# Kernel tuning notes

Hardware: AMD Instinct MI355X
Metric: run time of the kernel (lower is better)

Reference implementation:

```python
import jax, jax.numpy as jnp
import numpy as np

N_QUBITS = 14
N_TROTTER = 10
EVO_TIME = 1.0
BATCH = 2048
DIM = 2 ** N_QUBITS

# (-1)**bit_q(idx) for every basis index (Qiskit little-endian: qubit q <-> bit q)
_bits = (np.arange(DIM)[:, None] >> np.arange(N_QUBITS)[None, :]) & 1
_SIGNS = np.asarray(1 - 2 * _bits, dtype=np.float32)  # (DIM, n)


def _apply_1q(psi, U, q, n):
    A = 2 ** (n - 1 - q)
    B = 2 ** q
    psi = psi.reshape(A, 2, B)
    psi = jnp.einsum('ij,ajb->aib', U, psi)
    return psi.reshape(-1)


def _apply_zz(psi, theta, q, n):
    # CX(q,q+1); RZ(theta) on q+1; CX(q,q+1)  ==  diagonal exp(-i*theta/2 * Z_q Z_{q+1})
    A = 2 ** (n - 2 - q)
    B = 2 ** q
    em = jnp.exp(-0.5j * theta)
    ep = jnp.exp(0.5j * theta)
    diag = jnp.stack([em, ep, ep, em])  # axis index = 2*bit_{q+1} + bit_q
    psi = psi.reshape(A, 4, B) * diag[None, :, None]
    return psi.reshape(-1)


def _base_state(J, g):
    # Fixed part of the circuit (same for every sample): H on all qubits, then Trotter steps.
    n = N_QUBITS
    dt = EVO_TIME / N_TROTTER
    inv = 1.0 / np.sqrt(2.0)
    H = jnp.array([[inv, inv], [inv, -inv]], dtype=jnp.complex64)
    psi = jnp.zeros(DIM, dtype=jnp.complex64).at[0].set(1.0)
    for q in range(n):
        psi = _apply_1q(psi, H, q, n)
    for _ in range(N_TROTTER):
        for i in range(n - 1):
            psi = _apply_zz(psi, J[i] * dt, i, n)
        for i in range(n):
            half = 0.5 * g[i] * dt
            c = jnp.cos(half).astype(jnp.complex64)
            ms = -1j * jnp.sin(half)
            RX = jnp.stack([jnp.stack([c, ms]), jnp.stack([ms, c])])
            psi = _apply_1q(psi, RX, i, n)
    return psi


def _expectations(psi):
    # psi: (batch, DIM). Original observable order: block i -> qubit n-1-i, [X, Y, Z].
    n = N_QUBITS
    outs = []
    for i in range(n):
        q = n - 1 - i
        A = 2 ** (n - 1 - q)
        B = 2 ** q
        pr = psi.reshape(-1, A, 2, B)
        p0 = pr[:, :, 0, :]
        p1 = pr[:, :, 1, :]
        c = jnp.sum(jnp.conj(p0) * p1, axis=(1, 2))
        outs.append(2.0 * jnp.real(c))  # <X_q>
        outs.append(2.0 * jnp.imag(c))  # <Y_q>
        outs.append(jnp.sum(p0.real ** 2 + p0.imag ** 2 - p1.real ** 2 - p1.imag ** 2, axis=(1, 2)))  # <Z_q>
    return jnp.stack(outs, axis=1).astype(jnp.float32)


def setup_inputs() -> dict:
    key = jax.random.key(0)
    kx, kj, kg = jax.random.split(key, 3)
    x = jax.random.normal(kx, (BATCH, N_QUBITS), dtype=jnp.float32)
    J = jax.random.uniform(kj, (N_QUBITS - 1,), minval=0.5, maxval=1.5, dtype=jnp.float32)
    g = jax.random.uniform(kg, (N_QUBITS,), minval=0.5, maxval=1.5, dtype=jnp.float32)
    return {"x": x, "J": J, "g": g}


def reference(x, J, g):
    psi0 = _base_state(J, g)  # (DIM,), shared across the batch
    S = jnp.asarray(_SIGNS)   # (DIM, n)
    # Final per-sample RZ(x[b,q]) on qubit q -> diagonal phase exp(-i/2 * sum_q x_q * (-1)^bit_q)
    phase = jnp.exp((-0.5j) * (x @ S.T).astype(jnp.complex64))  # (batch, DIM)
    psi = psi0[None, :] * phase
    return _expectations(psi)
```

## Files before the change

### kernel.cpp

```cpp
#include <hip/hip_runtime.h>

#define NQ     14
#define DIMQ   16384
#define NWG    16
#define NTHR   256

typedef float vfloat4 __attribute__((ext_vector_type(4)));

struct Smem {
    float2 slab0[1024];
    float2 slab1[1024];
    float2 tabLo[64];
    float2 tabHi[128];
    float  red[48];
};

__device__ __forceinline__ void ld8v(const float2* p, float rb, float2 r[4]) {
    vfloat4 a, b;
    for (;;) {
        asm volatile("global_load_dwordx4 %0, %2, off sc0 sc1\n\t"
                     "global_load_dwordx4 %1, %2, off offset:16 sc0 sc1\n\t"
                     "s_waitcnt vmcnt(0)"
                     : "=&v"(a), "=&v"(b) : "v"(p) : "memory");
        float m0 = fminf(fminf(a.x * rb, a.y * rb), fminf(a.z * rb, a.w * rb));
        float m1 = fminf(fminf(b.x * rb, b.y * rb), fminf(b.z * rb, b.w * rb));
        bool ok = fminf(m0, m1) > 8.0f;
        if (__ballot(!ok) == 0ull) break;
        __builtin_amdgcn_s_sleep(1);
    }
    r[0] = make_float2(a.x - rb, a.y - rb); r[1] = make_float2(a.z - rb, a.w - rb);
    r[2] = make_float2(b.x - rb, b.y - rb); r[3] = make_float2(b.z - rb, b.w - rb);
}
__device__ __forceinline__ float2 d2f2(double d) { union { double d; float2 f; } u; u.d = d; return u.f; }
__device__ __forceinline__ double f22d(float2 f) { union { double d; float2 f; } u; u.f = f; return u.d; }
__device__ __forceinline__ void st2b(float2* p, float2 v, float wb) {
    float2 e = make_float2(v.x + wb, v.y + wb);
    asm volatile("global_store_dwordx2 %0, %1, off sc0 sc1"
                 : : "v"(p), "v"(f22d(e)) : "memory");
}
__device__ __forceinline__ void st8b(float2* p, const float2 r[4], float wb) {
    vfloat4 a, b;
    a.x = r[0].x + wb; a.y = r[0].y + wb; a.z = r[1].x + wb; a.w = r[1].y + wb;
    b.x = r[2].x + wb; b.y = r[2].y + wb; b.z = r[3].x + wb; b.w = r[3].y + wb;
    asm volatile("global_store_dwordx4 %0, %1, off sc0 sc1\n\t"
                 "global_store_dwordx4 %0, %2, off offset:16 sc0 sc1"
                 : : "v"(p), "v"(a), "v"(b) : "memory");
}
__device__ __forceinline__ void stfb(float* p, float v, float wb) {
    float e = v + wb;
    asm volatile("global_store_dword %0, %1, off sc0 sc1" : : "v"(p), "v"(e) : "memory");
}
__device__ __forceinline__ void ld3v(const float* p, float rb, bool use2,
                                     float& r0, float& r1, float& r2) {
    for (;;) {
        asm volatile("global_load_dword %0, %3, off sc0 sc1\n\t"
                     "global_load_dword %1, %3, off offset:1024 sc0 sc1\n\t"
                     "global_load_dword %2, %3, off offset:2048 sc0 sc1\n\t"
                     "s_waitcnt vmcnt(0)"
                     : "=&v"(r0), "=&v"(r1), "=&v"(r2) : "v"(p) : "memory");
        float m = fminf(r0 * rb, r1 * rb);
        if (use2) m = fminf(m, r2 * rb);
        bool ok = m > 8.0f;
        if (__ballot(!ok) == 0ull) break;
        __builtin_amdgcn_s_sleep(1);
    }
    r0 -= rb; r1 -= rb; r2 -= rb;
}

__device__ __forceinline__ float2 cmulf(float2 a, float2 b) {
    return make_float2(a.x * b.x - a.y * b.y, a.x * b.y + a.y * b.x);
}
__device__ __forceinline__ void bfly(float2& p0, float2& p1, float c, float s) {
    float2 n0 = make_float2(c * p0.x + s * p1.y, c * p0.y - s * p1.x);
    float2 n1 = make_float2(c * p1.x + s * p0.y, c * p1.y - s * p0.x);
    p0 = n0; p1 = n1;
}
__device__ __forceinline__ void bfly_shfl(float2& p, int mask, float c, float s) {
    float qx = __shfl_xor(p.x, mask);
    float qy = __shfl_xor(p.y, mask);
    p = make_float2(c * p.x + s * qy, c * p.y - s * qx);
}
__device__ __forceinline__ void zz_apply(const Smem& sm, float2& a, int k) {
    int d = (k ^ (k >> 1)) & 0x1FFF;
    float2 rot = cmulf(sm.tabLo[d & 63], sm.tabHi[d >> 6]);
    a = cmulf(a, rot);
}
__device__ __forceinline__ void stage_12(float2* slab, float2 r[4], int t) {
#pragma unroll
    for (int j = 0; j < 4; ++j) slab[(t << 2) | j] = r[j];
    __syncthreads();
#pragma unroll
    for (int j = 0; j < 4; ++j) r[j] = slab[t | (j << 8)];
}
__device__ __forceinline__ void stage_21(float2* slab, float2 r[4], int t) {
#pragma unroll
    for (int j = 0; j < 4; ++j) slab[t | (j << 8)] = r[j];
    __syncthreads();
#pragma unroll
    for (int j = 0; j < 4; ++j) r[j] = slab[(t << 2) | j];
}
__device__ __forceinline__ void reduce_qubit(const float2* slab, float* red,
                                             int sb, int i, int t) {
    float cr = 0.f, ci = 0.f, z = 0.f;
#pragma unroll
    for (int j = 0; j < 4; ++j) {
        const int m = (t << 2) | j;
        const float2 a = slab[m];
        const float n = a.x * a.x + a.y * a.y;
        if ((m >> sb) & 1) {
            z -= n;
        } else {
            z += n;
            const float2 b = slab[m ^ (1 << sb)];
            cr += a.x * b.x + a.y * b.y;
            ci += a.x * b.y - a.y * b.x;
        }
    }
#pragma unroll
    for (int off = 32; off; off >>= 1) {
        cr += __shfl_down(cr, off);
        ci += __shfl_down(ci, off);
        z  += __shfl_down(z, off);
    }
    if ((t & 63) == 0) {
        atomicAdd(&red[3 * i + 0], cr);
        atomicAdd(&red[3 * i + 1], ci);
        atomicAdd(&red[3 * i + 2], z);
    }
}

template <bool FIRST>
__device__ void phaseA(Smem& sm, float2* slab, float2* psi, int w, int t,
                       const float* c, const float* s, float rb, float wb) {
    float2 r[4];
    if (FIRST) {
#pragma unroll
        for (int j = 0; j < 4; ++j) r[j] = make_float2(0.0078125f, 0.0f);
    } else {
        ld8v(&psi[(w << 10) | (t << 2)], rb, r);
#pragma unroll
        for (int b = 2; b < 6; ++b) {
#pragma unroll
            for (int j = 0; j < 4; ++j) bfly_shfl(r[j], 1 << b, c[2 + b], s[2 + b]);
        }
    }
#pragma unroll
    for (int j = 0; j < 4; ++j) zz_apply(sm, r[j], (w << 10) | (t << 2) | j);
    bfly(r[0], r[1], c[0], s[0]); bfly(r[2], r[3], c[0], s[0]);
    bfly(r[0], r[2], c[1], s[1]); bfly(r[1], r[3], c[1], s[1]);
#pragma unroll
    for (int b = 0; b < 6; ++b) {
#pragma unroll
        for (int j = 0; j < 4; ++j) bfly_shfl(r[j], 1 << b, c[2 + b], s[2 + b]);
    }
    stage_12(slab, r, t);
    bfly(r[0], r[1], c[8], s[8]); bfly(r[2], r[3], c[8], s[8]);
    bfly(r[0], r[2], c[9], s[9]); bfly(r[1], r[3], c[9], s[9]);
#pragma unroll
    for (int j = 0; j < 4; ++j) st2b(&psi[(w << 10) | t | (j << 8)], r[j], wb);
}

template <bool KEEPSLAB>
__device__ void phaseB(Smem& sm, float2* s12, float2* s21, float2* psi,
                       int w, int t, const float* c, const float* s,
                       float rb, float wb) {
    float2 r[4];
    const int kbase = ((t >> 2) << 8) | (w << 4) | ((t & 3) << 2);
    ld8v(&psi[kbase], rb, r);
#pragma unroll
    for (int j = 0; j < 4; ++j) bfly_shfl(r[j], 16, c[10], s[10]);
#pragma unroll
    for (int j = 0; j < 4; ++j) bfly_shfl(r[j], 32, c[11], s[11]);
    stage_12(s12, r, t);
    bfly(r[0], r[1], c[12], s[12]); bfly(r[2], r[3], c[12], s[12]);
    bfly(r[0], r[2], c[13], s[13]); bfly(r[1], r[3], c[13], s[13]);
#pragma unroll
    for (int j = 0; j < 4; ++j) {
        const int m = t | (j << 8);
        zz_apply(sm, r[j], ((m >> 4) << 8) | (w << 4) | (m & 15));
    }
    bfly(r[0], r[1], c[12], s[12]); bfly(r[2], r[3], c[12], s[12]);
    bfly(r[0], r[2], c[13], s[13]); bfly(r[1], r[3], c[13], s[13]);
#pragma unroll
    for (int b = 0; b < 4; ++b) {
#pragma unroll
        for (int j = 0; j < 4; ++j) bfly_shfl(r[j], 1 << b, c[b], s[b]);
    }
#pragma unroll
    for (int j = 0; j < 4; ++j) bfly_shfl(r[j], 16, c[8], s[8]);
#pragma unroll
    for (int j = 0; j < 4; ++j) bfly_shfl(r[j], 32, c[9], s[9]);
    stage_21(s21, r, t);
#pragma unroll
    for (int j = 0; j < 4; ++j) bfly_shfl(r[j], 16, c[10], s[10]);
#pragma unroll
    for (int j = 0; j < 4; ++j) bfly_shfl(r[j], 32, c[11], s[11]);
    st8b(&psi[kbase], r, wb);
    if (KEEPSLAB) {
#pragma unroll
        for (int j = 0; j < 4; ++j) s21[(t << 2) | j] = r[j];
    }
}

extern "C" __global__ void __launch_bounds__(NTHR)
qr_all(const float* __restrict__ x, const float* __restrict__ J,
       const float* __restrict__ g, float* __restrict__ out,
       float2* __restrict__ psi, float* __restrict__ P) {
    __shared__ Smem sm;
    const int w = blockIdx.x;
    const int t = threadIdx.x;
    const float dt = 0.1f;

    if (t < 64) {
        float phi = 0.0f;
        for (int i = 0; i < 6; ++i) {
            const float h = 0.5f * J[i] * dt;
            phi += ((t >> i) & 1) ? h : -h;
        }
        float sn, cs; __sincosf(phi, &sn, &cs);
        sm.tabLo[t] = make_float2(cs, sn);
    } else if (t < 192) {
        const int v = t - 64;
        float phi = 0.0f;
        for (int i = 0; i < 7; ++i) {
            const float h = 0.5f * J[6 + i] * dt;
            phi += ((v >> i) & 1) ? h : -h;
        }
        float sn, cs; __sincosf(phi, &sn, &cs);
        sm.tabHi[v] = make_float2(cs, sn);
    }
    if (t < 48) sm.red[t] = 0.0f;
    float cc[NQ], ss[NQ];
#pragma unroll
    for (int i = 0; i < NQ; ++i) __sincosf(0.5f * g[i] * dt, &ss[i], &cc[i]);
    __syncthreads();

    phaseA<true>(sm, sm.slab0, psi, w, t, cc, ss, 0.0f, -4.0f);

    float esn[7], ecs[7];
#pragma unroll
    for (int k = 0; k < 7; ++k) {
        const int task = w * NTHR + t + (k << 12);
        const int b = task / NQ;
        const int i = task - b * NQ;
        __sincosf(x[b * NQ + 13 - i], &esn[k], &ecs[k]);
    }

#pragma unroll 1
    for (int sstep = 1; sstep <= 9; ++sstep) {
        const float wb = ((sstep + 1) & 1) ? -4.0f : 4.0f;
        const float rb = -wb;
        if (sstep & 1) {
            const int i21 = ((sstep - 1) >> 1) & 1;
            float2* s21 = i21 ? sm.slab1 : sm.slab0;
            float2* s12 = i21 ? sm.slab0 : sm.slab1;
            if (sstep == 9) {
                phaseB<true>(sm, s12, s21, psi, w, t, cc, ss, rb, wb);
                __syncthreads();
#pragma unroll
                for (int q = 0; q <= 3; ++q) reduce_qubit(sm.slab0, sm.red, q, 13 - q, t);
#pragma unroll
                for (int q = 8; q <= 13; ++q) reduce_qubit(sm.slab0, sm.red, q - 4, 13 - q, t);
            } else {
                phaseB<false>(sm, s12, s21, psi, w, t, cc, ss, rb, wb);
            }
        } else {
            float2* slab = ((sstep >> 1) & 1) ? sm.slab1 : sm.slab0;
            phaseA<false>(sm, slab, psi, w, t, cc, ss, rb, wb);
        }
    }

    {
        float2 r[4];
        ld8v(&psi[(w << 10) | (t << 2)], 4.0f, r);
#pragma unroll
        for (int b = 2; b < 6; ++b) {
#pragma unroll
            for (int j = 0; j < 4; ++j) bfly_shfl(r[j], 1 << b, cc[2 + b], ss[2 + b]);
        }
#pragma unroll
        for (int j = 0; j < 4; ++j) sm.slab1[(t << 2) | j] = r[j];
        __syncthreads();
#pragma unroll
        for (int q = 4; q <= 7; ++q) reduce_qubit(sm.slab1, sm.red, q, 13 - q, t);
        __syncthreads();
        if (t < 42) stfb(&P[t * NWG + w], sm.red[t], -4.0f);
    }

    float* sumbuf = (float*)sm.slab0;
    {
        float r0, r1, r2;
        ld3v(&P[t], -4.0f, t < 160, r0, r1, r2);
        sumbuf[t] = r0; sumbuf[t + 256] = r1; sumbuf[t + 512] = r2;
    }
    __syncthreads();
    float cv = 0.0f;
    if (t < 42) {
#pragma unroll
        for (int k = 0; k < NWG; ++k) cv += sumbuf[t * NWG + k];
    }
    __syncthreads();
    if (t < 42) sm.red[t] = cv;
    __syncthreads();

#pragma unroll
    for (int k = 0; k < 7; ++k) {
        const int task = w * NTHR + t + (k << 12);
        const int b = task / NQ;
        const int i = task - b * NQ;
        const float cr = sm.red[3 * i + 0];
        const float ci = sm.red[3 * i + 1];
        const float zz = sm.red[3 * i + 2];
        float* o = out + b * (3 * NQ) + 3 * i;
        o[0] = 2.0f * (ecs[k] * cr - esn[k] * ci);
        o[1] = 2.0f * (esn[k] * cr + ecs[k] * ci);
        o[2] = zz;
    }
}

extern "C" void kernel_launch(void* const* d_in, const int* in_sizes, int n_in,
                              void* d_out, int out_size, void* d_ws, size_t ws_size,
                              hipStream_t stream) {
    const float* x = (const float*)d_in[0];
    const float* J = (const float*)d_in[1];
    const float* g = (const float*)d_in[2];
    float* out = (float*)d_out;
    char* ws   = (char*)d_ws;
    float2* psi = (float2*)ws;
    float*  P   = (float*)(ws + DIMQ * sizeof(float2));
    (void)in_sizes; (void)n_in; (void)out_size; (void)ws_size;

    hipLaunchKernelGGL(qr_all, dim3(NWG), dim3(NTHR), 0, stream,
                       x, J, g, out, psi, P);
}
```

Measured before the change: 93.12 us.

## Pad LDS slabs to avoid bank conflicts and drop sc0 from global accesses

Adds one padding element every 8 entries in the shared-memory slabs so the transpose-style stage exchanges and reductions no longer hit the same LDS banks. Global loads and stores used for cross-workgroup flag polling and data exchange drop the sc0 bit and keep only sc1, changing the cache coherence scope. This is meant to cut LDS conflict stalls and the latency of the inter-workgroup handoff. The risk is stale data, since polling loads may now hit a non-coherent cache level, and LDS use grows slightly.

After: 93.17 us. About the same (+0.1%).

```diff
diff --git a/kernel.cpp b/kernel.cpp
--- a/kernel.cpp
+++ b/kernel.cpp
@@ -7,9 +7,11 @@
 
 typedef float vfloat4 __attribute__((ext_vector_type(4)));
 
+__device__ __forceinline__ int phys(int m) { return m + (m >> 3); }
+
 struct Smem {
-    float2 slab0[1024];
-    float2 slab1[1024];
+    float2 slab0[1152];
+    float2 slab1[1152];
     float2 tabLo[64];
     float2 tabHi[128];
     float  red[48];
@@ -18,8 +20,8 @@
 __device__ __forceinline__ void ld8v(const float2* p, float rb, float2 r[4]) {
     vfloat4 a, b;
     for (;;) {
-        asm volatile("global_load_dwordx4 %0, %2, off sc0 sc1\n\t"
-                     "global_load_dwordx4 %1, %2, off offset:16 sc0 sc1\n\t"
+        asm volatile("global_load_dwordx4 %0, %2, off sc1\n\t"
+                     "global_load_dwordx4 %1, %2, off offset:16 sc1\n\t"
                      "s_waitcnt vmcnt(0)"
                      : "=&v"(a), "=&v"(b) : "v"(p) : "memory");
         float m0 = fminf(fminf(a.x * rb, a.y * rb), fminf(a.z * rb, a.w * rb));
@@ -35,27 +37,27 @@
 __device__ __forceinline__ double f22d(float2 f) { union { double d; float2 f; } u; u.f = f; return u.d; }
 __device__ __forceinline__ void st2b(float2* p, float2 v, float wb) {
     float2 e = make_float2(v.x + wb, v.y + wb);
-    asm volatile("global_store_dwordx2 %0, %1, off sc0 sc1"
+    asm volatile("global_store_dwordx2 %0, %1, off sc1"
                  : : "v"(p), "v"(f22d(e)) : "memory");
 }
 __device__ __forceinline__ void st8b(float2* p, const float2 r[4], float wb) {
     vfloat4 a, b;
     a.x = r[0].x + wb; a.y = r[0].y + wb; a.z = r[1].x + wb; a.w = r[1].y + wb;
     b.x = r[2].x + wb; b.y = r[2].y + wb; b.z = r[3].x + wb; b.w = r[3].y + wb;
-    asm volatile("global_store_dwordx4 %0, %1, off sc0 sc1\n\t"
-                 "global_store_dwordx4 %0, %2, off offset:16 sc0 sc1"
+    asm volatile("global_store_dwordx4 %0, %1, off sc1\n\t"
+                 "global_store_dwordx4 %0, %2, off offset:16 sc1"
                  : : "v"(p), "v"(a), "v"(b) : "memory");
 }
 __device__ __forceinline__ void stfb(float* p, float v, float wb) {
     float e = v + wb;
-    asm volatile("global_store_dword %0, %1, off sc0 sc1" : : "v"(p), "v"(e) : "memory");
+    asm volatile("global_store_dword %0, %1, off sc1" : : "v"(p), "v"(e) : "memory");
 }
 __device__ __forceinline__ void ld3v(const float* p, float rb, bool use2,
                                      float& r0, float& r1, float& r2) {
     for (;;) {
-        asm volatile("global_load_dword %0, %3, off sc0 sc1\n\t"
-                     "global_load_dword %1, %3, off offset:1024 sc0 sc1\n\t"
-                     "global_load_dword %2, %3, off offset:2048 sc0 sc1\n\t"
+        asm volatile("global_load_dword %0, %3, off sc1\n\t"
+                     "global_load_dword %1, %3, off offset:1024 sc1\n\t"
+                     "global_load_dword %2, %3, off offset:2048 sc1\n\t"
                      "s_waitcnt vmcnt(0)"
                      : "=&v"(r0), "=&v"(r1), "=&v"(r2) : "v"(p) : "memory");
         float m = fminf(r0 * rb, r1 * rb);
@@ -87,17 +89,17 @@
 }
 __device__ __forceinline__ void stage_12(float2* slab, float2 r[4], int t) {
 #pragma unroll
-    for (int j = 0; j < 4; ++j) slab[(t << 2) | j] = r[j];
-    __syncthreads();
-#pragma unroll
-    for (int j = 0; j < 4; ++j) r[j] = slab[t | (j << 8)];
+    for (int j = 0; j < 4; ++j) slab[phys((t << 2) | j)] = r[j];
+    __syncthreads();
+#pragma unroll
+    for (int j = 0; j < 4; ++j) r[j] = slab[phys(t | (j << 8))];
 }
 __device__ __forceinline__ void stage_21(float2* slab, float2 r[4], int t) {
 #pragma unroll
-    for (int j = 0; j < 4; ++j) slab[t | (j << 8)] = r[j];
-    __syncthreads();
-#pragma unroll
-    for (int j = 0; j < 4; ++j) r[j] = slab[(t << 2) | j];
+    for (int j = 0; j < 4; ++j) slab[phys(t | (j << 8))] = r[j];
+    __syncthreads();
+#pragma unroll
+    for (int j = 0; j < 4; ++j) r[j] = slab[phys((t << 2) | j)];
 }
 __device__ __forceinline__ void reduce_qubit(const float2* slab, float* red,
                                              int sb, int i, int t) {
@@ -105,13 +107,13 @@
 #pragma unroll
     for (int j = 0; j < 4; ++j) {
         const int m = (t << 2) | j;
-        const float2 a = slab[m];
+        const float2 a = slab[phys(m)];
         const float n = a.x * a.x + a.y * a.y;
         if ((m >> sb) & 1) {
             z -= n;
         } else {
             z += n;
-            const float2 b = slab[m ^ (1 << sb)];
+            const float2 b = slab[phys(m ^ (1 << sb))];
             cr += a.x * b.x + a.y * b.y;
             ci += a.x * b.y - a.y * b.x;
         }
@@ -198,7 +200,7 @@
     st8b(&psi[kbase], r, wb);
     if (KEEPSLAB) {
 #pragma unroll
-        for (int j = 0; j < 4; ++j) s21[(t << 2) | j] = r[j];
+        for (int j = 0; j < 4; ++j) s21[phys((t << 2) | j)] = r[j];
     }
 }
 
@@ -279,7 +281,7 @@
             for (int j = 0; j < 4; ++j) bfly_shfl(r[j], 1 << b, cc[2 + b], ss[2 + b]);
         }
 #pragma unroll
-        for (int j = 0; j < 4; ++j) sm.slab1[(t << 2) | j] = r[j];
+        for (int j = 0; j < 4; ++j) sm.slab1[phys((t << 2) | j)] = r[j];
         __syncthreads();
 #pragma unroll
         for (int q = 4; q <= 7; ++q) reduce_qubit(sm.slab1, sm.red, q, 13 - q, t);
```
